# Kernel optimization log

Hardware: AMD Instinct MI355X
Metric: run time of the kernel (lower is better)

Reference implementation:

```python
import jax, jax.numpy as jnp
import numpy as np

B, L, R, E, D = 16, 28, 64, 34, 512


def setup_inputs() -> dict:
    key = jax.random.key(0)
    ks = jax.random.split(key, 10)
    logits = jax.random.uniform(ks[0], (B, L, R), dtype=jnp.float32)
    evt_embeddings = jax.random.normal(ks[1], (B, 1, D), dtype=jnp.float32)
    arg_embeddings = jax.random.normal(ks[2], (B, L, D), dtype=jnp.float32)
    # valid-arg counts in [1, L] (used as mask-count multiplier and divisor)
    arg_padding_num = jax.random.randint(ks[3], (B,), 1, L + 1).astype(jnp.float32)
    evt_type_list = jax.random.randint(ks[4], (B,), 0, E)
    s = 1.0 / np.sqrt(D)
    WRT = jax.random.normal(ks[5], (R, D, D), dtype=jnp.float32) * s
    WTT = jax.random.normal(ks[6], (E, D, D), dtype=jnp.float32) * s
    w1 = jax.random.normal(ks[7], (D, 64), dtype=jnp.float32) * s
    b1 = jnp.zeros((64,), dtype=jnp.float32)
    w2 = jax.random.normal(ks[8], (64, 1), dtype=jnp.float32) * (1.0 / 8.0)
    b2 = jnp.zeros((1,), dtype=jnp.float32)
    return {"logits": logits, "evt_embeddings": evt_embeddings,
            "arg_embeddings": arg_embeddings, "arg_padding_num": arg_padding_num,
            "evt_type_list": evt_type_list, "WRT": WRT, "WTT": WTT,
            "w1": w1, "b1": b1, "w2": w2, "b2": b2}


def reference(logits, evt_embeddings, arg_embeddings, arg_padding_num,
              evt_type_list, WRT, WTT, w1, b1, w2, b2):
    # role transition matrix per (event, arg): one-hot/soft select over WRT
    # [B,L,R] x [R,D,D] -> [B,L,D,D]  (dominant, memory-bound intermediate)
    role_mats = jnp.einsum('blr,rde->blde', logits, WRT)
    # event transition matrix: one-hot select over WTT == gather
    evt_mats = WTT[evt_type_list]                      # [B,D,D]
    # event embedding transform: [B,1,D] bmm [B,D,D] -> [B,D]
    evt_trans = jnp.einsum('bd,bde->be', evt_embeddings[:, 0, :], evt_mats)
    # per-arg transform: [B,L,D] bmm [B,L,D,D] -> [B,L,D]
    role_trans = jnp.einsum('bld,blde->ble', arg_embeddings, role_mats)
    # multiply by count, sum over args, divide by count (as in the original)
    role_trans = role_trans * arg_padding_num[:, None, None]
    new_sum = jnp.sum(role_trans, axis=1)              # [B,D]
    div = new_sum / arg_padding_num[:, None]
    graph_embeddings = (div + evt_trans) / 2.0         # [B,D]
    # scorer MLP: Linear(D,64) -> ReLU -> Linear(64,1) -> Sigmoid
    h = jax.nn.relu(graph_embeddings @ w1 + b1)
    score = jax.nn.sigmoid(h @ w2 + b2)                # [B,1]
    return score
```

## Files before the change

### kernel.cpp

```cpp
#include <hip/hip_runtime.h>
#include <math.h>

#define BB 16
#define LL 28
#define RR 64
#define DD 512
#define NROLE 512
#define NEVT  256
#define F4RR  65536

__global__ void __launch_bounds__(256, 2) kernel_a(
    const float* __restrict__ logits,
    const float* __restrict__ arg,
    const float* __restrict__ WRT,
    const float* __restrict__ WTT,
    const float* __restrict__ evt_emb,
    const int*   __restrict__ evt_type,
    float* __restrict__ part,
    float* __restrict__ evt_part)
{
    __shared__ float smem[8192];
    const int t   = threadIdx.x;
    const int bid = blockIdx.x;

    if (bid < NROLE) {
        const int rid = bid;
        const int rp  = rid >> 4;
        const int d0  = ((rid >> 1) & 7) * 64;
        const int eh  = rid & 1;

        const float4* WBase = (const float4*)(WRT + ((size_t)(2 * rp) * DD + d0) * DD);

        const int e4    = t & 63;
        const int h     = t >> 6;
        const int co    = eh * 64 + e4;
        const int kbase = 16 * h;

        float4 w[8];
#pragma unroll
        for (int i = 0; i < 8; ++i)
            w[i] = WBase[(size_t)(kbase + i) * 128 + co];

        {
            const int b  = t >> 4;
            const int d4 = t & 15;
            const float4* ap = (const float4*)(arg) + (size_t)(b * LL) * 128 + (d0 >> 2) + d4;
            const float2* lp = (const float2*)(logits) + (size_t)(b * LL) * 32 + rp;
            float4 g0 = {0.f,0.f,0.f,0.f}, g1 = {0.f,0.f,0.f,0.f};
#pragma unroll 7
            for (int l = 0; l < LL; ++l) {
                const float4 av = ap[(size_t)l * 128];
                const float2 lg = lp[(size_t)l * 32];
                g0.x = fmaf(lg.x, av.x, g0.x); g0.y = fmaf(lg.x, av.y, g0.y);
                g0.z = fmaf(lg.x, av.z, g0.z); g0.w = fmaf(lg.x, av.w, g0.w);
                g1.x = fmaf(lg.y, av.x, g1.x); g1.y = fmaf(lg.y, av.y, g1.y);
                g1.z = fmaf(lg.y, av.z, g1.z); g1.w = fmaf(lg.y, av.w, g1.w);
            }
            const int row = 4 * d4;
            smem[       (row + 0) * 16 + b] = g0.x;
            smem[       (row + 1) * 16 + b] = g0.y;
            smem[       (row + 2) * 16 + b] = g0.z;
            smem[       (row + 3) * 16 + b] = g0.w;
            smem[1024 + (row + 0) * 16 + b] = g1.x;
            smem[1024 + (row + 1) * 16 + b] = g1.y;
            smem[1024 + (row + 2) * 16 + b] = g1.z;
            smem[1024 + (row + 3) * 16 + b] = g1.w;
        }
        __syncthreads();

        float4 acc[16];
#pragma unroll
        for (int i = 0; i < 16; ++i) acc[i] = make_float4(0.f, 0.f, 0.f, 0.f);

        for (int mb = 0; mb < 4; ++mb) {
            const int mbn = (mb + 1) & 3;
            const size_t nb = (size_t)(mbn >> 1) * F4RR;
            const int kn = kbase + (mbn & 1) * 8;
            float4 wn[8];
#pragma unroll
            for (int i = 0; i < 8; ++i)
                wn[i] = WBase[nb + (size_t)(kn + i) * 128 + co];

            const float* Gr = smem + (mb >> 1) * 1024;
            const int k0 = kbase + (mb & 1) * 8;
#pragma unroll
            for (int i = 0; i < 8; ++i) {
                const float* gp = Gr + (k0 + i) * 16;
                const float4 ga = ((const float4*)gp)[0];
                const float4 gb = ((const float4*)gp)[1];
                const float4 gc = ((const float4*)gp)[2];
                const float4 gd = ((const float4*)gp)[3];
#define ACC(j, S) \
                acc[j].x = fmaf(S, w[i].x, acc[j].x); \
                acc[j].y = fmaf(S, w[i].y, acc[j].y); \
                acc[j].z = fmaf(S, w[i].z, acc[j].z); \
                acc[j].w = fmaf(S, w[i].w, acc[j].w);
                ACC(0,  ga.x) ACC(1,  ga.y) ACC(2,  ga.z) ACC(3,  ga.w)
                ACC(4,  gb.x) ACC(5,  gb.y) ACC(6,  gb.z) ACC(7,  gb.w)
                ACC(8,  gc.x) ACC(9,  gc.y) ACC(10, gc.z) ACC(11, gc.w)
                ACC(12, gd.x) ACC(13, gd.y) ACC(14, gd.z) ACC(15, gd.w)
#undef ACC
            }
#pragma unroll
            for (int i = 0; i < 8; ++i) w[i] = wn[i];
        }

        __syncthreads();
        float4* cb = (float4*)smem;
        if (h >= 2) {
#pragma unroll
            for (int i = 0; i < 16; ++i)
                cb[(h - 2) * 1024 + i * 64 + e4] = acc[i];
        }
        __syncthreads();
        if (h < 2) {
#pragma unroll
            for (int i = 0; i < 16; ++i) {
                const float4 v = cb[h * 1024 + i * 64 + e4];
                acc[i].x += v.x; acc[i].y += v.y; acc[i].z += v.z; acc[i].w += v.w;
            }
        }
        __syncthreads();
        if (h == 1) {
#pragma unroll
            for (int i = 0; i < 16; ++i)
                cb[i * 64 + e4] = acc[i];
        }
        __syncthreads();
        if (h == 0) {
            float4* po = (float4*)part + (size_t)rid * 1024;
#pragma unroll
            for (int i = 0; i < 16; ++i) {
                const float4 v = cb[i * 64 + e4];
                acc[i].x += v.x; acc[i].y += v.y; acc[i].z += v.z; acc[i].w += v.w;
                po[i * 64 + e4] = acc[i];
            }
        }
    } else {
        const int cid = bid - NROLE;
        const int b   = cid >> 4;
        const int dc  = cid & 15;
        const int d0  = dc * 32;
        const int ty  = evt_type[b];
        const float* Wt = WTT + (size_t)ty * DD * DD;
        const int e4 = t & 127;
        const int s  = t >> 7;
        float4 a = {0.f, 0.f, 0.f, 0.f};
#pragma unroll
        for (int db = 0; db < 32; db += 16) {
            float  em[8];
            float4 wv[8];
#pragma unroll
            for (int i = 0; i < 8; ++i) {
                const int d = d0 + db + s + 2 * i;
                em[i] = evt_emb[b * DD + d];
                wv[i] = ((const float4*)(Wt + (size_t)d * DD))[e4];
            }
#pragma unroll
            for (int i = 0; i < 8; ++i) {
                a.x = fmaf(em[i], wv[i].x, a.x);
                a.y = fmaf(em[i], wv[i].y, a.y);
                a.z = fmaf(em[i], wv[i].z, a.z);
                a.w = fmaf(em[i], wv[i].w, a.w);
            }
        }
        float4* sm4 = (float4*)smem;
        if (s == 1) sm4[e4] = a;
        __syncthreads();
        if (s == 0) {
            const float4 q4 = sm4[e4];
            a.x += q4.x; a.y += q4.y; a.z += q4.z; a.w += q4.w;
            ((float4*)evt_part)[(size_t)cid * 128 + e4] = a;
        }
    }
}

__global__ void __launch_bounds__(1024) kernel_tail(
    const float* __restrict__ part,
    const float* __restrict__ evt_part,
    const float* __restrict__ w1,
    const float* __restrict__ b1,
    const float* __restrict__ w2,
    const float* __restrict__ b2,
    float* __restrict__ out)
{
    __shared__ float4 sm4[2048];
    __shared__ float  gsm[512];
    __shared__ float  hred[1024];
    const int b  = blockIdx.x;
    const int t  = threadIdx.x;
    const int e4 = t & 127;
    const int g  = t >> 7;
    const int eh = e4 >> 6;
    const int ec = e4 & 63;

    const float4* p4  = (const float4*)part;
    const float4* e4p = (const float4*)evt_part;
    float4 s = {0.f, 0.f, 0.f, 0.f};
#pragma unroll
    for (int i = 0; i < 32; ++i) {
        const int m = g * 32 + i;
        const float4 v = p4[(size_t)(2 * m + eh) * 1024 + b * 64 + ec];
        s.x += v.x; s.y += v.y; s.z += v.z; s.w += v.w;
    }
    sm4[g * 128 + e4] = s;
    float4 es = {0.f, 0.f, 0.f, 0.f};
#pragma unroll
    for (int i = 0; i < 2; ++i) {
        const int dc = g * 2 + i;
        const float4 v = e4p[(size_t)(b * 16 + dc) * 128 + e4];
        es.x += v.x; es.y += v.y; es.z += v.z; es.w += v.w;
    }
    sm4[1024 + g * 128 + e4] = es;
    __syncthreads();

    if (t < 128) {
        float4 dv = {0.f,0.f,0.f,0.f}, ev = {0.f,0.f,0.f,0.f};
#pragma unroll
        for (int q = 0; q < 8; ++q) {
            const float4 a = sm4[q * 128 + t];
            const float4 c = sm4[1024 + q * 128 + t];
            dv.x += a.x; dv.y += a.y; dv.z += a.z; dv.w += a.w;
            ev.x += c.x; ev.y += c.y; ev.z += c.z; ev.w += c.w;
        }
        float4 gr;
        gr.x = (dv.x + ev.x) * 0.5f;
        gr.y = (dv.y + ev.y) * 0.5f;
        gr.z = (dv.z + ev.z) * 0.5f;
        gr.w = (dv.w + ev.w) * 0.5f;
        ((float4*)gsm)[t] = gr;
    }
    __syncthreads();

    {
        const int j  = t & 63;
        const int dq = t >> 6;
        float hp = 0.f;
#pragma unroll 8
        for (int i = 0; i < 32; ++i) {
            const int d = dq * 32 + i;
            hp = fmaf(gsm[d], w1[d * 64 + j], hp);
        }
        hred[t] = hp;
    }
    __syncthreads();
    if (t < 64) {
        float hh = b1[t];
#pragma unroll
        for (int q = 0; q < 16; ++q) hh += hred[q * 64 + t];
        hh = fmaxf(hh, 0.f);
        float v = hh * w2[t];
#pragma unroll
        for (int off = 32; off > 0; off >>= 1) v += __shfl_down(v, off, 64);
        if (t == 0) out[b] = 1.f / (1.f + expf(-(v + b2[0])));
    }
}

extern "C" void kernel_launch(void* const* d_in, const int* in_sizes, int n_in,
                              void* d_out, int out_size, void* d_ws, size_t ws_size,
                              hipStream_t stream) {
    const float* logits   = (const float*)d_in[0];
    const float* evt_emb  = (const float*)d_in[1];
    const float* arg_emb  = (const float*)d_in[2];
    const int*   evt_type = (const int*)d_in[4];
    const float* WRT      = (const float*)d_in[5];
    const float* WTT      = (const float*)d_in[6];
    const float* w1       = (const float*)d_in[7];
    const float* b1       = (const float*)d_in[8];
    const float* w2       = (const float*)d_in[9];
    const float* b2       = (const float*)d_in[10];
    float* out = (float*)d_out;

    float* part     = (float*)d_ws;
    float* evt_part = part + (size_t)NROLE * 4096;

    hipLaunchKernelGGL(kernel_a, dim3(NROLE + NEVT), dim3(256), 0, stream,
                       logits, arg_emb, WRT, WTT, evt_emb, evt_type, part, evt_part);
    hipLaunchKernelGGL(kernel_tail, dim3(BB), dim3(1024), 0, stream,
                       part, evt_part, w1, b1, w2, b2, out);
}
```

Measured before the change: 149.0 us.

## Fuse tail reduction and MLP into main kernel via atomic-ticket last-block scheme

Merges the two-kernel pipeline into one launch. The last-arriving blocks, chosen by an atomic ticket counter, spin-wait for all blocks and then perform the cross-block reduction, which is now spread over 136 blocks instead of 16. The final 16 tickets then run the MLP, and role and event blocks are interleaved in the block index order. The aim is to remove the second launch and to parallelise the tail reduction. The cost is a memset launch, spin-waits that depend on forward progress of blocks already resident, and extra fences.

```diff
diff --git a/kernel.cpp b/kernel.cpp
--- a/kernel.cpp
+++ b/kernel.cpp
@@ -7,24 +7,37 @@
 #define DD 512
 #define NROLE 512
 #define NEVT  256
+#define NBLK  (NROLE + NEVT)
+#define NRED  136
+#define NMLP  16
 #define F4RR  65536
 
-__global__ void __launch_bounds__(256, 2) kernel_a(
+__global__ void __launch_bounds__(256, 2) kernel_fused(
     const float* __restrict__ logits,
     const float* __restrict__ arg,
     const float* __restrict__ WRT,
     const float* __restrict__ WTT,
     const float* __restrict__ evt_emb,
     const int*   __restrict__ evt_type,
+    const float* __restrict__ w1,
+    const float* __restrict__ b1,
+    const float* __restrict__ w2,
+    const float* __restrict__ b2,
     float* __restrict__ part,
-    float* __restrict__ evt_part)
+    float* __restrict__ evt_part,
+    float* __restrict__ div_acc,
+    float* __restrict__ evt_acc,
+    unsigned* __restrict__ ctrs,
+    float* __restrict__ out)
 {
     __shared__ float smem[8192];
+    __shared__ unsigned s_tick;
     const int t   = threadIdx.x;
-    const int bid = blockIdx.x;
-
-    if (bid < NROLE) {
-        const int rid = bid;
+    const int q   = blockIdx.x / 3;
+    const int rem = blockIdx.x - 3 * q;
+
+    if (rem != 2) {
+        const int rid = 2 * q + rem;
         const int rp  = rid >> 4;
         const int d0  = ((rid >> 1) & 7) * 64;
         const int eh  = rid & 1;
@@ -137,7 +150,7 @@
             }
         }
     } else {
-        const int cid = bid - NROLE;
+        const int cid = q;
         const int b   = cid >> 4;
         const int dc  = cid & 15;
         const int d0  = dc * 32;
@@ -173,86 +186,105 @@
             ((float4*)evt_part)[(size_t)cid * 128 + e4] = a;
         }
     }
-}
-
-__global__ void __launch_bounds__(1024) kernel_tail(
-    const float* __restrict__ part,
-    const float* __restrict__ evt_part,
-    const float* __restrict__ w1,
-    const float* __restrict__ b1,
-    const float* __restrict__ w2,
-    const float* __restrict__ b2,
-    float* __restrict__ out)
-{
-    __shared__ float4 sm4[2048];
-    __shared__ float  gsm[512];
-    __shared__ float  hred[1024];
-    const int b  = blockIdx.x;
-    const int t  = threadIdx.x;
-    const int e4 = t & 127;
-    const int g  = t >> 7;
-    const int eh = e4 >> 6;
-    const int ec = e4 & 63;
-
-    const float4* p4  = (const float4*)part;
-    const float4* e4p = (const float4*)evt_part;
-    float4 s = {0.f, 0.f, 0.f, 0.f};
-#pragma unroll
-    for (int i = 0; i < 32; ++i) {
-        const int m = g * 32 + i;
-        const float4 v = p4[(size_t)(2 * m + eh) * 1024 + b * 64 + ec];
-        s.x += v.x; s.y += v.y; s.z += v.z; s.w += v.w;
+
+    __threadfence();
+    __syncthreads();
+    if (t == 0)
+        s_tick = __hip_atomic_fetch_add(&ctrs[0], 1u, __ATOMIC_RELEASE,
+                                        __HIP_MEMORY_SCOPE_AGENT);
+    __syncthreads();
+    {
+        const unsigned tick = s_tick;
+        if (tick < (unsigned)(NBLK - NRED)) return;
+        const int ridx = (int)tick - (NBLK - NRED);
+        if (t == 0) {
+            while (__hip_atomic_load(&ctrs[0], __ATOMIC_ACQUIRE,
+                                     __HIP_MEMORY_SCOPE_AGENT) < (unsigned)NBLK)
+                __builtin_amdgcn_s_sleep(8);
+        }
+        __syncthreads();
+        __threadfence();
+
+        if (ridx < 128) {
+            float4* sred = (float4*)smem;
+            const int oo = t & 15;
+            const int pg = t >> 4;
+            const int o4 = ridx * 16 + oo;
+            const int b  = o4 >> 7;
+            const int e4g = o4 & 127;
+            const int eh = e4g >> 6;
+            const int ec = e4g & 63;
+            const float4* p4 = (const float4*)part;
+            float4 s = {0.f, 0.f, 0.f, 0.f};
+#pragma unroll 8
+            for (int i = 0; i < 16; ++i) {
+                const int m = pg * 16 + i;
+                const float4 v = p4[(size_t)(2 * m + eh) * 1024 + b * 64 + ec];
+                s.x += v.x; s.y += v.y; s.z += v.z; s.w += v.w;
+            }
+            sred[pg * 16 + oo] = s;
+            __syncthreads();
+            if (t < 16) {
+                float4 tot = sred[t];
+#pragma unroll
+                for (int g = 1; g < 16; ++g) {
+                    const float4 v = sred[g * 16 + t];
+                    tot.x += v.x; tot.y += v.y; tot.z += v.z; tot.w += v.w;
+                }
+                ((float4*)div_acc)[ridx * 16 + t] = tot;
+            }
+        } else {
+            const int o4 = (ridx - 128) * 256 + t;
+            const int b  = o4 >> 7;
+            const int el = o4 & 127;
+            const float4* e4p = (const float4*)evt_part;
+            float4 s = {0.f, 0.f, 0.f, 0.f};
+#pragma unroll
+            for (int dc = 0; dc < 16; ++dc) {
+                const float4 v = e4p[(size_t)(b * 16 + dc) * 128 + el];
+                s.x += v.x; s.y += v.y; s.z += v.z; s.w += v.w;
+            }
+            ((float4*)evt_acc)[o4] = s;
+        }
     }
-    sm4[g * 128 + e4] = s;
-    float4 es = {0.f, 0.f, 0.f, 0.f};
-#pragma unroll
-    for (int i = 0; i < 2; ++i) {
-        const int dc = g * 2 + i;
-        const float4 v = e4p[(size_t)(b * 16 + dc) * 128 + e4];
-        es.x += v.x; es.y += v.y; es.z += v.z; es.w += v.w;
-    }
-    sm4[1024 + g * 128 + e4] = es;
+
+    __threadfence();
     __syncthreads();
-
-    if (t < 128) {
-        float4 dv = {0.f,0.f,0.f,0.f}, ev = {0.f,0.f,0.f,0.f};
-#pragma unroll
-        for (int q = 0; q < 8; ++q) {
-            const float4 a = sm4[q * 128 + t];
-            const float4 c = sm4[1024 + q * 128 + t];
-            dv.x += a.x; dv.y += a.y; dv.z += a.z; dv.w += a.w;
-            ev.x += c.x; ev.y += c.y; ev.z += c.z; ev.w += c.w;
-        }
-        float4 gr;
-        gr.x = (dv.x + ev.x) * 0.5f;
-        gr.y = (dv.y + ev.y) * 0.5f;
-        gr.z = (dv.z + ev.z) * 0.5f;
-        gr.w = (dv.w + ev.w) * 0.5f;
-        ((float4*)gsm)[t] = gr;
-    }
+    if (t == 0)
+        s_tick = __hip_atomic_fetch_add(&ctrs[1], 1u, __ATOMIC_RELEASE,
+                                        __HIP_MEMORY_SCOPE_AGENT);
     __syncthreads();
-
     {
+        const unsigned tick2 = s_tick;
+        if (tick2 < (unsigned)(NRED - NMLP)) return;
+        const int b = (int)tick2 - (NRED - NMLP);
+        if (t == 0) {
+            while (__hip_atomic_load(&ctrs[1], __ATOMIC_ACQUIRE,
+                                     __HIP_MEMORY_SCOPE_AGENT) < (unsigned)NRED)
+                __builtin_amdgcn_s_sleep(8);
+        }
+        __syncthreads();
+        __threadfence();
+
         const int j  = t & 63;
         const int dq = t >> 6;
         float hp = 0.f;
 #pragma unroll 8
-        for (int i = 0; i < 32; ++i) {
-            const int d = dq * 32 + i;
-            hp = fmaf(gsm[d], w1[d * 64 + j], hp);
-        }
-        hred[t] = hp;
-    }
-    __syncthreads();
-    if (t < 64) {
-        float hh = b1[t];
-#pragma unroll
-        for (int q = 0; q < 16; ++q) hh += hred[q * 64 + t];
-        hh = fmaxf(hh, 0.f);
-        float v = hh * w2[t];
-#pragma unroll
-        for (int off = 32; off > 0; off >>= 1) v += __shfl_down(v, off, 64);
-        if (t == 0) out[b] = 1.f / (1.f + expf(-(v + b2[0])));
+        for (int i = 0; i < 128; ++i) {
+            const int d = dq * 128 + i;
+            const float g = (div_acc[b * DD + d] + evt_acc[b * DD + d]) * 0.5f;
+            hp = fmaf(g, w1[d * 64 + j], hp);
+        }
+        smem[t] = hp;
+        __syncthreads();
+        if (t < 64) {
+            float hh = b1[j] + smem[j] + smem[64 + j] + smem[128 + j] + smem[192 + j];
+            hh = fmaxf(hh, 0.f);
+            float v = hh * w2[j];
+#pragma unroll
+            for (int off = 32; off > 0; off >>= 1) v += __shfl_down(v, off, 64);
+            if (j == 0) out[b] = 1.f / (1.f + expf(-(v + b2[0])));
+        }
     }
 }
 
@@ -273,9 +305,13 @@
 
     float* part     = (float*)d_ws;
     float* evt_part = part + (size_t)NROLE * 4096;
-
-    hipLaunchKernelGGL(kernel_a, dim3(NROLE + NEVT), dim3(256), 0, stream,
-                       logits, arg_emb, WRT, WTT, evt_emb, evt_type, part, evt_part);
-    hipLaunchKernelGGL(kernel_tail, dim3(BB), dim3(1024), 0, stream,
-                       part, evt_part, w1, b1, w2, b2, out);
+    float* div_acc  = evt_part + (size_t)NEVT * DD;
+    float* evt_acc  = div_acc + BB * DD;
+    unsigned* ctrs  = (unsigned*)(evt_acc + BB * DD);
+
+    hipMemsetAsync(ctrs, 0, 2 * sizeof(unsigned), stream);
+    hipLaunchKernelGGL(kernel_fused, dim3(NBLK), dim3(256), 0, stream,
+                       logits, arg_emb, WRT, WTT, evt_emb, evt_type,
+                       w1, b1, w2, b2, part, evt_part, div_acc, evt_acc,
+                       ctrs, out);
 }
```

After: 365.6 us. +145.4%, slower.
